# Kernel optimization log

Measured on AMD Instinct MI355X. Metric: run time of the kernel, lower is better.

## Reference

```python
import jax, jax.numpy as jnp
import numpy as np

D_MODEL = 1024
NUM_HEADS = 16
D_K = D_MODEL // NUM_HEADS
B, S = 4, 2048


def setup_inputs() -> dict:
    key = jax.random.key(0)
    ks = jax.random.split(key, 11)
    scale = 1.0 / np.sqrt(D_MODEL)
    inp = {
        'query': jax.random.normal(ks[0], (B, S, D_MODEL), dtype=jnp.float32),
        'key':   jax.random.normal(ks[1], (B, S, D_MODEL), dtype=jnp.float32),
        'value': jax.random.normal(ks[2], (B, S, D_MODEL), dtype=jnp.float32),
        'Wq': jax.random.normal(ks[3], (D_MODEL, D_MODEL), dtype=jnp.float32) * scale,
        'bq': jnp.zeros((D_MODEL,), dtype=jnp.float32),
        'Wk': jax.random.normal(ks[4], (D_MODEL, D_MODEL), dtype=jnp.float32) * scale,
        'bk': jnp.zeros((D_MODEL,), dtype=jnp.float32),
        'Wv': jax.random.normal(ks[5], (D_MODEL, D_MODEL), dtype=jnp.float32) * scale,
        'bv': jnp.zeros((D_MODEL,), dtype=jnp.float32),
        'Wo': jax.random.normal(ks[6], (D_MODEL, D_MODEL), dtype=jnp.float32) * scale,
        'bo': jnp.zeros((D_MODEL,), dtype=jnp.float32),
    }
    return inp


def reference(query, key, value, Wq, bq, Wk, bk, Wv, bv, Wo, bo):
    b, sq, _ = query.shape
    sk = key.shape[1]
    # projections (torch Linear: x @ W.T + b; here W stored as [in, out])
    Q = query @ Wq + bq
    K = key @ Wk + bk
    V = value @ Wv + bv
    # split heads: [b, h, s, d_k]
    Q = Q.reshape(b, sq, NUM_HEADS, D_K).transpose(0, 2, 1, 3)
    K = K.reshape(b, sk, NUM_HEADS, D_K).transpose(0, 2, 1, 3)
    V = V.reshape(b, sk, NUM_HEADS, D_K).transpose(0, 2, 1, 3)
    # scaled dot-product attention (full [b,h,sq,sk] scores, as in source)
    scores = jnp.einsum('bhqd,bhkd->bhqk', Q, K) / jnp.sqrt(jnp.float32(D_K))
    attn = jax.nn.softmax(scores, axis=-1)
    out = jnp.einsum('bhqk,bhkd->bhqd', attn, V)
    out = out.transpose(0, 2, 1, 3).reshape(b, sq, D_MODEL)
    return out @ Wo + bo
```

## Files before the change

### kernel.cpp

```cpp
#include <hip/hip_runtime.h>
#include <hip/hip_bf16.h>
#include <stdint.h>

typedef __bf16 bf16x8 __attribute__((ext_vector_type(8)));
typedef __bf16 bf16x4 __attribute__((ext_vector_type(4)));
typedef float  f32x4  __attribute__((ext_vector_type(4)));
typedef unsigned short u16;

#define D_MODEL 1024
#define NUM_HEADS 16
#define DK 64
#define BATCH 4
#define SEQ 2048
#define M_TOTAL (BATCH*SEQ)
#define QK_SCALE 0.18033688011112042f

static __device__ __forceinline__ u16 f2bf(float f) {
    __bf16 h = (__bf16)f;
    return __builtin_bit_cast(u16, h);
}

#define ASYNC16(gptr, lptr) __builtin_amdgcn_global_load_lds( \
    (const __attribute__((address_space(1))) unsigned*)(uintptr_t)(gptr), \
    (__attribute__((address_space(3))) unsigned*)(unsigned)(uintptr_t)(lptr), 16, 0, 0)

__global__ void detect_dtype(const u16* __restrict__ q, unsigned* __restrict__ flag) {
    __shared__ int sh[256];
    int cnt = 0;
    for (int i = threadIdx.x; i < 8192; i += 256) {
        u16 v = q[2 * i];
        int e = (v >> 7) & 0xFF;
        if (e >= 100 && e <= 134) cnt++;
    }
    sh[threadIdx.x] = cnt;
    __syncthreads();
    for (int s = 128; s > 0; s >>= 1) {
        if (threadIdx.x < s) sh[threadIdx.x] += sh[threadIdx.x + s];
        __syncthreads();
    }
    if (threadIdx.x == 0) *flag = (sh[0] > 4096) ? 1u : 0u;
}

__global__ void transpose_w(const u16* __restrict__ W0, const u16* __restrict__ W1,
                            const u16* __restrict__ W2, const u16* __restrict__ W3,
                            u16* __restrict__ WT, const unsigned* __restrict__ flagp) {
    __shared__ u16 tile[32][33];
    const u16* W = (blockIdx.z == 0) ? W0 : (blockIdx.z == 1) ? W1 : (blockIdx.z == 2) ? W2 : W3;
    u16* T = WT + (size_t)blockIdx.z * D_MODEL * D_MODEL;
    bool is_bf16 = (*flagp != 0);
    int x = threadIdx.x, y0 = threadIdx.y;
    int bx = blockIdx.x * 32, by = blockIdx.y * 32;
    if (is_bf16) {
#pragma unroll
        for (int i = 0; i < 4; i++) {
            int y = y0 + i * 8;
            tile[y][x] = W[(size_t)(by + y) * D_MODEL + bx + x];
        }
    } else {
        const float* Wf = (const float*)W;
#pragma unroll
        for (int i = 0; i < 4; i++) {
            int y = y0 + i * 8;
            tile[y][x] = f2bf(Wf[(size_t)(by + y) * D_MODEL + bx + x]);
        }
    }
    __syncthreads();
#pragma unroll
    for (int i = 0; i < 4; i++) {
        int y = y0 + i * 8;
        T[(size_t)(bx + y) * D_MODEL + by + x] = tile[x][y];
    }
}

__global__ __launch_bounds__(256) void gemm_qkv(
    const u16* __restrict__ qin, const u16* __restrict__ kin, const u16* __restrict__ vin,
    const u16* __restrict__ WT,
    const u16* __restrict__ bq, const u16* __restrict__ bk, const u16* __restrict__ bv,
    u16* __restrict__ Qp, u16* __restrict__ Kp, u16* __restrict__ VpT,
    const unsigned* __restrict__ flagp)
{
    __shared__ __align__(16) u16 As[128 * 32];
    __shared__ __align__(16) u16 Bs[128 * 32];
    const int id  = blockIdx.x;
    const int xcd = id & 7, j = id >> 3;
    const int zy  = xcd * 24 + (j >> 3);
    const int bx  = j & 7;
    const int z   = zy >> 6, by = zy & 63;

    const u16* A    = (z == 0) ? qin : (z == 1) ? kin : vin;
    const u16* W    = WT + (size_t)z * 1048576;
    const u16* bias = (z == 0) ? bq : (z == 1) ? bk : bv;
    u16* C          = (z == 0) ? Qp : (z == 1) ? Kp : VpT;
    const int transV = (z == 2);
    const float oscale = (z == 0) ? QK_SCALE : 1.0f;

    const int tid  = threadIdx.x;
    const int lane = tid & 63, w = tid >> 6;
    const int quad = lane >> 4, l15 = lane & 15;
    const int wm = w >> 1, wn = w & 1;
    const int m_blk = by * 128, n_blk = bx * 128;
    const bool is_bf16 = (*flagp != 0);

    f32x4 acc[4][4] = {};

    const int ch0 = w * 2, ch1 = w * 2 + 1;
    const int sr0 = ch0 * 16 + (lane >> 2), sr1 = ch1 * 16 + (lane >> 2);
    const int skp = (lane & 3) * 8;
    const int frow = tid >> 1, fkp = (tid & 1) * 16;
    const float* Af = (const float*)A;

    for (int k0 = 0; k0 < D_MODEL; k0 += 32) {
        if (!is_bf16) {
            const float* src = Af + (size_t)(m_blk + frow) * D_MODEL + k0 + fkp;
            float4 f0 = ((const float4*)src)[0];
            float4 f1 = ((const float4*)src)[1];
            float4 f2 = ((const float4*)src)[2];
            float4 f3 = ((const float4*)src)[3];
            bf16x8 p0, p1;
            p0[0] = (__bf16)f0.x; p0[1] = (__bf16)f0.y; p0[2] = (__bf16)f0.z; p0[3] = (__bf16)f0.w;
            p0[4] = (__bf16)f1.x; p0[5] = (__bf16)f1.y; p0[6] = (__bf16)f1.z; p0[7] = (__bf16)f1.w;
            p1[0] = (__bf16)f2.x; p1[1] = (__bf16)f2.y; p1[2] = (__bf16)f2.z; p1[3] = (__bf16)f2.w;
            p1[4] = (__bf16)f3.x; p1[5] = (__bf16)f3.y; p1[6] = (__bf16)f3.z; p1[7] = (__bf16)f3.w;
            *(bf16x8*)&As[frow * 32 + fkp]     = p0;
            *(bf16x8*)&As[frow * 32 + fkp + 8] = p1;
        } else {
            ASYNC16(A + (size_t)(m_blk + sr0) * D_MODEL + k0 + skp, &As[ch0 * 512]);
            ASYNC16(A + (size_t)(m_blk + sr1) * D_MODEL + k0 + skp, &As[ch1 * 512]);
        }
        ASYNC16(W + (size_t)(n_blk + sr0) * D_MODEL + k0 + skp, &Bs[ch0 * 512]);
        ASYNC16(W + (size_t)(n_blk + sr1) * D_MODEL + k0 + skp, &Bs[ch1 * 512]);
        __syncthreads();

        bf16x8 af[4], bg[4];
#pragma unroll
        for (int sm = 0; sm < 4; sm++)
            af[sm] = *(const bf16x8*)&As[(wm * 64 + sm * 16 + l15) * 32 + quad * 8];
#pragma unroll
        for (int sn = 0; sn < 4; sn++)
            bg[sn] = *(const bf16x8*)&Bs[(wn * 64 + sn * 16 + l15) * 32 + quad * 8];
#pragma unroll
        for (int sm = 0; sm < 4; sm++)
#pragma unroll
            for (int sn = 0; sn < 4; sn++)
                acc[sm][sn] = __builtin_amdgcn_mfma_f32_16x16x32_bf16(af[sm], bg[sn], acc[sm][sn], 0, 0, 0);
        __syncthreads();
    }

#pragma unroll
    for (int sn = 0; sn < 4; sn++) {
        int n = n_blk + wn * 64 + sn * 16 + l15;
        float bvf = is_bf16 ? (float)((const __bf16*)bias)[n] : ((const float*)bias)[n];
#pragma unroll
        for (int sm = 0; sm < 4; sm++) {
            int mrow = m_blk + wm * 64 + sm * 16 + quad * 4;
            if (transV) {
                int b = mrow >> 11, s = mrow & 2047;
                ushort4 pk;
                pk.x = f2bf(acc[sm][sn][0] + bvf);
                pk.y = f2bf(acc[sm][sn][1] + bvf);
                pk.z = f2bf(acc[sm][sn][2] + bvf);
                pk.w = f2bf(acc[sm][sn][3] + bvf);
                *(ushort4*)(C + (size_t)b * D_MODEL * SEQ + (size_t)n * SEQ + s) = pk;
            } else {
#pragma unroll
                for (int r = 0; r < 4; r++)
                    C[(size_t)(mrow + r) * D_MODEL + n] = f2bf((acc[sm][sn][r] + bvf) * oscale);
            }
        }
    }
}

__global__ __launch_bounds__(256) void gemm_o(
    const u16* __restrict__ A, const u16* __restrict__ WT,
    const u16* __restrict__ bias, u16* __restrict__ C,
    const unsigned* __restrict__ flagp)
{
    __shared__ __align__(16) u16 As[64 * 32];
    __shared__ __align__(16) u16 Bs[128 * 32];
    const int id  = blockIdx.x;
    const int xcd = id & 7, j = id >> 3;
    const int by  = xcd * 16 + (j >> 3);
    const int bx  = j & 7;

    const int tid  = threadIdx.x;
    const int lane = tid & 63, w = tid >> 6;
    const int quad = lane >> 4, l15 = lane & 15;
    const int wm = w >> 1, wn = w & 1;
    const int m_blk = by * 64, n_blk = bx * 128;
    const bool is_bf16 = (*flagp != 0);

    f32x4 acc[2][4] = {};
    const int srow = lane >> 2, skp = (lane & 3) * 8;

    for (int k0 = 0; k0 < D_MODEL; k0 += 32) {
#pragma unroll
        for (int i = 0; i < 3; i++) {
            int c = w * 3 + i;
            if (c < 4)
                ASYNC16(A  + (size_t)(m_blk + c * 16 + srow) * D_MODEL + k0 + skp, &As[c * 512]);
            else
                ASYNC16(WT + (size_t)(n_blk + (c - 4) * 16 + srow) * D_MODEL + k0 + skp, &Bs[(c - 4) * 512]);
        }
        __syncthreads();

        bf16x8 af[2], bg[4];
#pragma unroll
        for (int sm = 0; sm < 2; sm++)
            af[sm] = *(const bf16x8*)&As[(wm * 32 + sm * 16 + l15) * 32 + quad * 8];
#pragma unroll
        for (int sn = 0; sn < 4; sn++)
            bg[sn] = *(const bf16x8*)&Bs[(wn * 64 + sn * 16 + l15) * 32 + quad * 8];
#pragma unroll
        for (int sm = 0; sm < 2; sm++)
#pragma unroll
            for (int sn = 0; sn < 4; sn++)
                acc[sm][sn] = __builtin_amdgcn_mfma_f32_16x16x32_bf16(af[sm], bg[sn], acc[sm][sn], 0, 0, 0);
        __syncthreads();
    }

#pragma unroll
    for (int sn = 0; sn < 4; sn++) {
        int n = n_blk + wn * 64 + sn * 16 + l15;
        float bvf = is_bf16 ? (float)((const __bf16*)bias)[n] : ((const float*)bias)[n];
#pragma unroll
        for (int sm = 0; sm < 2; sm++) {
            int mrow = m_blk + wm * 32 + sm * 16 + quad * 4;
            if (!is_bf16) {
                float* Cf = (float*)C;
#pragma unroll
                for (int r = 0; r < 4; r++)
                    Cf[(size_t)(mrow + r) * D_MODEL + n] = acc[sm][sn][r] + bvf;
            } else {
#pragma unroll
                for (int r = 0; r < 4; r++)
                    C[(size_t)(mrow + r) * D_MODEL + n] = f2bf(acc[sm][sn][r] + bvf);
            }
        }
    }
}

__global__ __launch_bounds__(256) void attn_kernel(
    const u16* __restrict__ Qp, const u16* __restrict__ Kp,
    const u16* __restrict__ VpT, u16* __restrict__ AO)
{
    __shared__ __align__(16) u16 Ks[2][64 * 64];
    __shared__ __align__(16) u16 Vs[2][64 * 64];
    __shared__ __align__(16) u16 Ps[4][32][68];
    const int id  = blockIdx.x;
    const int xcd = id & 7, j = id >> 3;
    const int bh  = xcd * 8 + (j >> 4);
    const int qx  = j & 15;

    const int tid  = threadIdx.x;
    const int lane = tid & 63, w = tid >> 6;
    const int quad = lane >> 4, l15 = lane & 15;
    const int b = bh >> 4, h = bh & 15;
    const int q_base = qx * 128 + w * 32;

    bf16x8 bQ[2][2];
#pragma unroll
    for (int sn = 0; sn < 2; sn++)
#pragma unroll
        for (int ds = 0; ds < 2; ds++)
            bQ[sn][ds] = *(const bf16x8*)(Qp + (size_t)(b * SEQ + q_base + sn * 16 + l15) * D_MODEL
                                              + h * DK + ds * 32 + quad * 8);

    float lsum[2] = {0.0f, 0.0f};
    f32x4 OT[2][4] = {};

    const u16* Kbase = Kp  + (size_t)(b * SEQ) * D_MODEL + h * DK;
    const u16* Vbase = VpT + (size_t)b * D_MODEL * SEQ + (size_t)(h * DK) * SEQ;

    const int c0   = w * 2;
    const int lrow = lane >> 3;
    const int ug   = (lane & 7) ^ lrow;
    const int swz  = l15 & 7;

    auto issue_tile = [&](int key0, int bf) {
#pragma unroll
        for (int i = 0; i < 2; i++) {
            int c = c0 + i;
            ASYNC16(Kbase + (size_t)(key0 + c * 8 + lrow) * D_MODEL + ug * 8, &Ks[bf][c * 512]);
            ASYNC16(Vbase + (size_t)(c * 8 + lrow) * SEQ + key0 + ug * 8,     &Vs[bf][c * 512]);
        }
    };

    issue_tile(0, 0);
    __syncthreads();

    for (int t = 0; t < SEQ / 64; t++) {
        const int cur = t & 1;
        if (t + 1 < SEQ / 64) issue_tile((t + 1) * 64, cur ^ 1);

#pragma unroll
        for (int kc = 0; kc < 4; kc++) {
            const int krow = (kc * 16 + l15) * 64;
            bf16x8 k0 = *(const bf16x8*)&Ks[cur][krow + ((quad ^ swz) * 8)];
            bf16x8 k1 = *(const bf16x8*)&Ks[cur][krow + (((4 + quad) ^ swz) * 8)];
#pragma unroll
            for (int sn = 0; sn < 2; sn++) {
                f32x4 s = {};
                s = __builtin_amdgcn_mfma_f32_16x16x32_bf16(k0, bQ[sn][0], s, 0, 0, 0);
                s = __builtin_amdgcn_mfma_f32_16x16x32_bf16(k1, bQ[sn][1], s, 0, 0, 0);
                float p0 = __builtin_amdgcn_exp2f(s[0]);
                float p1 = __builtin_amdgcn_exp2f(s[1]);
                float p2 = __builtin_amdgcn_exp2f(s[2]);
                float p3 = __builtin_amdgcn_exp2f(s[3]);
                lsum[sn] += (p0 + p1) + (p2 + p3);
                bf16x4 pk;
                pk[0] = (__bf16)p0; pk[1] = (__bf16)p1; pk[2] = (__bf16)p2; pk[3] = (__bf16)p3;
                *(bf16x4*)&Ps[w][sn * 16 + l15][kc * 16 + quad * 4] = pk;
            }
        }

#pragma unroll
        for (int kc2 = 0; kc2 < 2; kc2++) {
            bf16x8 bP0 = *(const bf16x8*)&Ps[w][l15][kc2 * 32 + quad * 8];
            bf16x8 bP1 = *(const bf16x8*)&Ps[w][16 + l15][kc2 * 32 + quad * 8];
#pragma unroll
            for (int nd = 0; nd < 4; nd++) {
                bf16x8 aV = *(const bf16x8*)&Vs[cur][(nd * 16 + l15) * 64
                                                    + (((kc2 * 4 + quad) ^ swz) * 8)];
                OT[0][nd] = __builtin_amdgcn_mfma_f32_16x16x32_bf16(aV, bP0, OT[0][nd], 0, 0, 0);
                OT[1][nd] = __builtin_amdgcn_mfma_f32_16x16x32_bf16(aV, bP1, OT[1][nd], 0, 0, 0);
            }
        }
        __syncthreads();
    }

#pragma unroll
    for (int sn = 0; sn < 2; sn++) {
        lsum[sn] += __shfl_xor(lsum[sn], 16, 64);
        lsum[sn] += __shfl_xor(lsum[sn], 32, 64);
        float rl = 1.0f / lsum[sn];
        size_t rowbase = (size_t)(b * SEQ + q_base + sn * 16 + l15) * D_MODEL + h * DK;
#pragma unroll
        for (int nd = 0; nd < 4; nd++) {
            ushort4 pk;
            pk.x = f2bf(OT[sn][nd][0] * rl);
            pk.y = f2bf(OT[sn][nd][1] * rl);
            pk.z = f2bf(OT[sn][nd][2] * rl);
            pk.w = f2bf(OT[sn][nd][3] * rl);
            *(ushort4*)(AO + rowbase + nd * 16 + quad * 4) = pk;
        }
    }
}

extern "C" void kernel_launch(void* const* d_in, const int* in_sizes, int n_in,
                              void* d_out, int out_size, void* d_ws, size_t ws_size,
                              hipStream_t stream) {
    const u16* q  = (const u16*)d_in[0];
    const u16* k  = (const u16*)d_in[1];
    const u16* v  = (const u16*)d_in[2];
    const u16* Wq = (const u16*)d_in[3];
    const u16* bq = (const u16*)d_in[4];
    const u16* Wk = (const u16*)d_in[5];
    const u16* bk = (const u16*)d_in[6];
    const u16* Wv = (const u16*)d_in[7];
    const u16* bv = (const u16*)d_in[8];
    const u16* Wo = (const u16*)d_in[9];
    const u16* bo = (const u16*)d_in[10];

    u16* ws   = (u16*)d_ws;
    unsigned* flagp = (unsigned*)ws;
    u16* WT   = ws + 16;
    u16* Qp   = WT + (size_t)4 * 1024 * 1024;
    u16* Kp   = Qp + (size_t)M_TOTAL * D_MODEL;
    u16* VpT  = Kp + (size_t)M_TOTAL * D_MODEL;
    u16* AO   = VpT + (size_t)M_TOTAL * D_MODEL;

    detect_dtype<<<1, 256, 0, stream>>>(q, flagp);
    transpose_w<<<dim3(32, 32, 4), dim3(32, 8), 0, stream>>>(Wq, Wk, Wv, Wo, WT, flagp);
    gemm_qkv<<<1536, 256, 0, stream>>>(q, k, v, WT, bq, bk, bv, Qp, Kp, VpT, flagp);
    attn_kernel<<<1024, 256, 0, stream>>>(Qp, Kp, VpT, AO);
    gemm_o<<<1024, 256, 0, stream>>>(AO, WT + 3 * 1048576, bo, (u16*)d_out, flagp);
}
```

Baseline: 417.7 us.

## Restructure QKV GEMM into 256x256 double-buffered ping-pong pipeline with swizzled LDS

Replaces the 128x128, single-buffered QKV projection GEMM with a 512-thread kernel that computes 256x256 output tiles. It uses a K-step of 64, double-buffered LDS with an XOR swizzle, and interleaves staging of the next tiles between quarter-blocks of MFMA work. Manual waitcnt/barrier control and s_setprio aim to overlap global loads with matrix math and raise operand reuse per LDS byte. The trade-offs are 128KB of LDS per block, which likely limits residency to one block per CU, and a 384-block grid that leaves an uneven final wave. The fp32 input path still converts synchronously in registers.

```diff
diff --git a/kernel.cpp b/kernel.cpp
--- a/kernel.cpp
+++ b/kernel.cpp
@@ -23,6 +23,9 @@
 #define ASYNC16(gptr, lptr) __builtin_amdgcn_global_load_lds( \
     (const __attribute__((address_space(1))) unsigned*)(uintptr_t)(gptr), \
     (__attribute__((address_space(3))) unsigned*)(unsigned)(uintptr_t)(lptr), 16, 0, 0)
+
+#define FENCE() asm volatile("" ::: "memory")
+#define BARRIER() do { FENCE(); __builtin_amdgcn_s_barrier(); FENCE(); } while (0)
 
 __global__ void detect_dtype(const u16* __restrict__ q, unsigned* __restrict__ flag) {
     __shared__ int sh[256];
@@ -72,99 +75,169 @@
     }
 }
 
-__global__ __launch_bounds__(256) void gemm_qkv(
+__global__ __launch_bounds__(512, 2) void gemm_qkv(
     const u16* __restrict__ qin, const u16* __restrict__ kin, const u16* __restrict__ vin,
     const u16* __restrict__ WT,
     const u16* __restrict__ bq, const u16* __restrict__ bk, const u16* __restrict__ bv,
     u16* __restrict__ Qp, u16* __restrict__ Kp, u16* __restrict__ VpT,
     const unsigned* __restrict__ flagp)
 {
-    __shared__ __align__(16) u16 As[128 * 32];
-    __shared__ __align__(16) u16 Bs[128 * 32];
+    __shared__ __align__(16) u16 As[2][256 * 64];
+    __shared__ __align__(16) u16 Bs[2][256 * 64];
+
+    const int KTILES = D_MODEL / 64;
+
     const int id  = blockIdx.x;
-    const int xcd = id & 7, j = id >> 3;
-    const int zy  = xcd * 24 + (j >> 3);
-    const int bx  = j & 7;
-    const int z   = zy >> 6, by = zy & 63;
+    const int wg  = (id & 7) * 48 + (id >> 3);
+    const int z   = wg >> 7;
+    const int rr  = wg & 127;
+    const int m_blk = (rr >> 2) * 256;
+    const int n_blk = (rr & 3) * 256;
 
     const u16* A    = (z == 0) ? qin : (z == 1) ? kin : vin;
     const u16* W    = WT + (size_t)z * 1048576;
     const u16* bias = (z == 0) ? bq : (z == 1) ? bk : bv;
     u16* C          = (z == 0) ? Qp : (z == 1) ? Kp : VpT;
-    const int transV = (z == 2);
     const float oscale = (z == 0) ? QK_SCALE : 1.0f;
+    const bool is_bf16 = (*flagp != 0);
+    const float* Af = (const float*)A;
 
     const int tid  = threadIdx.x;
     const int lane = tid & 63, w = tid >> 6;
     const int quad = lane >> 4, l15 = lane & 15;
-    const int wm = w >> 1, wn = w & 1;
-    const int m_blk = by * 128, n_blk = bx * 128;
-    const bool is_bf16 = (*flagp != 0);
-
-    f32x4 acc[4][4] = {};
-
-    const int ch0 = w * 2, ch1 = w * 2 + 1;
-    const int sr0 = ch0 * 16 + (lane >> 2), sr1 = ch1 * 16 + (lane >> 2);
-    const int skp = (lane & 3) * 8;
-    const int frow = tid >> 1, fkp = (tid & 1) * 16;
-    const float* Af = (const float*)A;
-
-    for (int k0 = 0; k0 < D_MODEL; k0 += 32) {
-        if (!is_bf16) {
-            const float* src = Af + (size_t)(m_blk + frow) * D_MODEL + k0 + fkp;
-            float4 f0 = ((const float4*)src)[0];
-            float4 f1 = ((const float4*)src)[1];
-            float4 f2 = ((const float4*)src)[2];
-            float4 f3 = ((const float4*)src)[3];
-            bf16x8 p0, p1;
-            p0[0] = (__bf16)f0.x; p0[1] = (__bf16)f0.y; p0[2] = (__bf16)f0.z; p0[3] = (__bf16)f0.w;
-            p0[4] = (__bf16)f1.x; p0[5] = (__bf16)f1.y; p0[6] = (__bf16)f1.z; p0[7] = (__bf16)f1.w;
-            p1[0] = (__bf16)f2.x; p1[1] = (__bf16)f2.y; p1[2] = (__bf16)f2.z; p1[3] = (__bf16)f2.w;
-            p1[4] = (__bf16)f3.x; p1[5] = (__bf16)f3.y; p1[6] = (__bf16)f3.z; p1[7] = (__bf16)f3.w;
-            *(bf16x8*)&As[frow * 32 + fkp]     = p0;
-            *(bf16x8*)&As[frow * 32 + fkp + 8] = p1;
-        } else {
-            ASYNC16(A + (size_t)(m_blk + sr0) * D_MODEL + k0 + skp, &As[ch0 * 512]);
-            ASYNC16(A + (size_t)(m_blk + sr1) * D_MODEL + k0 + skp, &As[ch1 * 512]);
-        }
-        ASYNC16(W + (size_t)(n_blk + sr0) * D_MODEL + k0 + skp, &Bs[ch0 * 512]);
-        ASYNC16(W + (size_t)(n_blk + sr1) * D_MODEL + k0 + skp, &Bs[ch1 * 512]);
-        __syncthreads();
-
-        bf16x8 af[4], bg[4];
-#pragma unroll
-        for (int sm = 0; sm < 4; sm++)
-            af[sm] = *(const bf16x8*)&As[(wm * 64 + sm * 16 + l15) * 32 + quad * 8];
-#pragma unroll
-        for (int sn = 0; sn < 4; sn++)
-            bg[sn] = *(const bf16x8*)&Bs[(wn * 64 + sn * 16 + l15) * 32 + quad * 8];
-#pragma unroll
-        for (int sm = 0; sm < 4; sm++)
-#pragma unroll
-            for (int sn = 0; sn < 4; sn++)
-                acc[sm][sn] = __builtin_amdgcn_mfma_f32_16x16x32_bf16(af[sm], bg[sn], acc[sm][sn], 0, 0, 0);
-        __syncthreads();
-    }
-
-#pragma unroll
-    for (int sn = 0; sn < 4; sn++) {
-        int n = n_blk + wn * 64 + sn * 16 + l15;
-        float bvf = is_bf16 ? (float)((const __bf16*)bias)[n] : ((const float*)bias)[n];
-#pragma unroll
-        for (int sm = 0; sm < 4; sm++) {
-            int mrow = m_blk + wm * 64 + sm * 16 + quad * 4;
-            if (transV) {
-                int b = mrow >> 11, s = mrow & 2047;
+    const int swz  = l15 & 7;
+    const int wm = w >> 2, wn = w & 3;
+
+    const int lrow = lane >> 3;
+    const int ug   = (lane & 7) ^ lrow;
+
+    auto stageA = [&](int t, int h) {
+        if (t >= KTILES) return;
+        u16* ldsbase = &As[t & 1][h * 8192];
+        const int k0 = t * 64;
+#pragma unroll
+        for (int i = 0; i < 2; i++) {
+            const int c   = w * 2 + i;
+            const int row = m_blk + h * 128 + c * 8 + lrow;
+            if (is_bf16) {
+                ASYNC16(A + (size_t)row * D_MODEL + k0 + ug * 8, ldsbase + c * 512);
+            } else {
+                const float* s = Af + (size_t)row * D_MODEL + k0 + ug * 8;
+                float4 f0 = ((const float4*)s)[0];
+                float4 f1 = ((const float4*)s)[1];
+                bf16x8 p;
+                p[0] = (__bf16)f0.x; p[1] = (__bf16)f0.y; p[2] = (__bf16)f0.z; p[3] = (__bf16)f0.w;
+                p[4] = (__bf16)f1.x; p[5] = (__bf16)f1.y; p[6] = (__bf16)f1.z; p[7] = (__bf16)f1.w;
+                *(bf16x8*)(ldsbase + c * 512 + lane * 8) = p;
+            }
+        }
+    };
+    auto stageB = [&](int t, int h) {
+        if (t >= KTILES) return;
+        u16* ldsbase = &Bs[t & 1][h * 8192];
+        const int k0 = t * 64;
+#pragma unroll
+        for (int i = 0; i < 2; i++) {
+            const int c   = w * 2 + i;
+            const int row = n_blk + h * 128 + c * 8 + lrow;
+            ASYNC16(W + (size_t)row * D_MODEL + k0 + ug * 8, ldsbase + c * 512);
+        }
+    };
+
+    f32x4 acc[8][4] = {};
+    bf16x8 a[4][2];
+    bf16x8 b[4][2];
+
+#define LOAD_A(MBASE) \
+    _Pragma("unroll") \
+    for (int mf = 0; mf < 4; mf++) \
+        _Pragma("unroll") \
+        for (int ks = 0; ks < 2; ks++) \
+            a[mf][ks] = *(const bf16x8*)&Abuf[(wm * 128 + (MBASE + mf) * 16 + l15) * 64 \
+                                              + (((ks * 4 + quad) ^ swz) * 8)];
+#define LOAD_B(NBASE) \
+    _Pragma("unroll") \
+    for (int nf = 0; nf < 2; nf++) \
+        _Pragma("unroll") \
+        for (int ks = 0; ks < 2; ks++) \
+            b[NBASE + nf][ks] = *(const bf16x8*)&Bbuf[(wn * 64 + (NBASE + nf) * 16 + l15) * 64 \
+                                                      + (((ks * 4 + quad) ^ swz) * 8)];
+#define MFMA_QUAD(MBASE, NBASE) \
+    __builtin_amdgcn_s_setprio(1); \
+    _Pragma("unroll") \
+    for (int mf = 0; mf < 4; mf++) \
+        _Pragma("unroll") \
+        for (int nf = 0; nf < 2; nf++) \
+            _Pragma("unroll") \
+            for (int ks = 0; ks < 2; ks++) \
+                acc[MBASE + mf][NBASE + nf] = __builtin_amdgcn_mfma_f32_16x16x32_bf16( \
+                    a[mf][ks], b[NBASE + nf][ks], acc[MBASE + mf][NBASE + nf], 0, 0, 0); \
+    __builtin_amdgcn_s_setprio(0);
+
+    stageB(0, 0); stageB(0, 1);
+    stageA(0, 0); stageA(0, 1);
+    stageB(1, 0); stageB(1, 1);
+    asm volatile("s_waitcnt vmcnt(4) lgkmcnt(0)" ::: "memory");
+    __builtin_amdgcn_s_barrier();
+    FENCE();
+
+#pragma unroll 1
+    for (int t = 0; t < KTILES; t++) {
+        const u16* Abuf = &As[t & 1][0];
+        const u16* Bbuf = &Bs[t & 1][0];
+
+        LOAD_A(0); LOAD_B(0);
+        stageA(t + 1, 0);
+        BARRIER();
+        asm volatile("s_waitcnt lgkmcnt(0)" ::: "memory");
+        MFMA_QUAD(0, 0);
+        BARRIER();
+
+        LOAD_B(2);
+        stageA(t + 1, 1);
+        BARRIER();
+        asm volatile("s_waitcnt lgkmcnt(0)" ::: "memory");
+        MFMA_QUAD(0, 2);
+        BARRIER();
+
+        LOAD_A(4);
+        stageB(t + 2, 0);
+        BARRIER();
+        asm volatile("s_waitcnt lgkmcnt(0)" ::: "memory");
+        MFMA_QUAD(4, 2);
+        BARRIER();
+
+        stageB(t + 2, 1);
+        BARRIER();
+        asm volatile("s_waitcnt lgkmcnt(0)" ::: "memory");
+        MFMA_QUAD(4, 0);
+        if (t == KTILES - 2)      { asm volatile("s_waitcnt vmcnt(0)" ::: "memory"); }
+        else if (t < KTILES - 2)  { asm volatile("s_waitcnt vmcnt(4)" ::: "memory"); }
+        BARRIER();
+    }
+#undef LOAD_A
+#undef LOAD_B
+#undef MFMA_QUAD
+
+#pragma unroll
+    for (int nf = 0; nf < 4; nf++) {
+        const int n = n_blk + wn * 64 + nf * 16 + l15;
+        const float bvf = is_bf16 ? (float)((const __bf16*)bias)[n] : ((const float*)bias)[n];
+#pragma unroll
+        for (int mf = 0; mf < 8; mf++) {
+            const int mrow = m_blk + wm * 128 + mf * 16 + quad * 4;
+            if (z == 2) {
+                const int bb = mrow >> 11, s = mrow & 2047;
                 ushort4 pk;
-                pk.x = f2bf(acc[sm][sn][0] + bvf);
-                pk.y = f2bf(acc[sm][sn][1] + bvf);
-                pk.z = f2bf(acc[sm][sn][2] + bvf);
-                pk.w = f2bf(acc[sm][sn][3] + bvf);
-                *(ushort4*)(C + (size_t)b * D_MODEL * SEQ + (size_t)n * SEQ + s) = pk;
+                pk.x = f2bf(acc[mf][nf][0] + bvf);
+                pk.y = f2bf(acc[mf][nf][1] + bvf);
+                pk.z = f2bf(acc[mf][nf][2] + bvf);
+                pk.w = f2bf(acc[mf][nf][3] + bvf);
+                *(ushort4*)(C + (size_t)bb * D_MODEL * SEQ + (size_t)n * SEQ + s) = pk;
             } else {
 #pragma unroll
                 for (int r = 0; r < 4; r++)
-                    C[(size_t)(mrow + r) * D_MODEL + n] = f2bf((acc[sm][sn][r] + bvf) * oscale);
+                    C[(size_t)(mrow + r) * D_MODEL + n] = f2bf((acc[mf][nf][r] + bvf) * oscale);
             }
         }
     }
@@ -371,7 +444,7 @@
 
     detect_dtype<<<1, 256, 0, stream>>>(q, flagp);
     transpose_w<<<dim3(32, 32, 4), dim3(32, 8), 0, stream>>>(Wq, Wk, Wv, Wo, WT, flagp);
-    gemm_qkv<<<1536, 256, 0, stream>>>(q, k, v, WT, bq, bk, bv, Qp, Kp, VpT, flagp);
+    gemm_qkv<<<384, 512, 0, stream>>>(q, k, v, WT, bq, bk, bv, Qp, Kp, VpT, flagp);
     attn_kernel<<<1024, 256, 0, stream>>>(Qp, Kp, VpT, AO);
     gemm_o<<<1024, 256, 0, stream>>>(AO, WT + 3 * 1048576, bo, (u16*)d_out, flagp);
 }
```

Result: slower. 443.2 us (+6.1%).

## Pre-convert fp32 activations to bf16 and widen QKV GEMM K-tile with swizzled LDS

Applied to the files above, without the earlier changes.

Adds a separate kernel that converts the fp32 q/k/v inputs to bf16 once, so the QKV GEMM can always use async global-to-LDS loads instead of doing in-loop fp32 loads and conversions. The GEMM K-step grows from 32 to 64 with an XOR-swizzled LDS layout meant to avoid bank conflicts, and the block-to-tile mapping is changed. The cost is an extra pass over the activations with a bf16 round-trip through memory; the conversion buffer is reused as the attention output buffer.

```diff
diff --git a/kernel.cpp b/kernel.cpp
--- a/kernel.cpp
+++ b/kernel.cpp
@@ -13,6 +13,7 @@
 #define BATCH 4
 #define SEQ 2048
 #define M_TOTAL (BATCH*SEQ)
+#define MD ((size_t)M_TOTAL * D_MODEL)
 #define QK_SCALE 0.18033688011112042f
 
 static __device__ __forceinline__ u16 f2bf(float f) {
@@ -39,6 +40,25 @@
         __syncthreads();
     }
     if (threadIdx.x == 0) *flag = (sh[0] > 4096) ? 1u : 0u;
+}
+
+__global__ __launch_bounds__(256) void convert_bf16(
+    const u16* __restrict__ q, const u16* __restrict__ k, const u16* __restrict__ v,
+    u16* __restrict__ CVT, const unsigned* __restrict__ flagp)
+{
+    if (*flagp != 0) return;
+    const int z = blockIdx.y;
+    const float* src = (const float*)((z == 0) ? q : (z == 1) ? k : v);
+    u16* dst = CVT + (size_t)z * MD;
+    const size_t stride = (size_t)gridDim.x * 256 * 8;
+    for (size_t base = ((size_t)blockIdx.x * 256 + threadIdx.x) * 8; base < MD; base += stride) {
+        float4 f0 = *(const float4*)(src + base);
+        float4 f1 = *(const float4*)(src + base + 4);
+        bf16x8 p;
+        p[0] = (__bf16)f0.x; p[1] = (__bf16)f0.y; p[2] = (__bf16)f0.z; p[3] = (__bf16)f0.w;
+        p[4] = (__bf16)f1.x; p[5] = (__bf16)f1.y; p[6] = (__bf16)f1.z; p[7] = (__bf16)f1.w;
+        *(bf16x8*)(dst + base) = p;
+    }
 }
 
 __global__ void transpose_w(const u16* __restrict__ W0, const u16* __restrict__ W1,
@@ -74,97 +94,92 @@
 
 __global__ __launch_bounds__(256) void gemm_qkv(
     const u16* __restrict__ qin, const u16* __restrict__ kin, const u16* __restrict__ vin,
-    const u16* __restrict__ WT,
+    const u16* __restrict__ CVT, const u16* __restrict__ WT,
     const u16* __restrict__ bq, const u16* __restrict__ bk, const u16* __restrict__ bv,
     u16* __restrict__ Qp, u16* __restrict__ Kp, u16* __restrict__ VpT,
     const unsigned* __restrict__ flagp)
 {
-    __shared__ __align__(16) u16 As[128 * 32];
-    __shared__ __align__(16) u16 Bs[128 * 32];
+    __shared__ __align__(16) u16 As[128 * 64];
+    __shared__ __align__(16) u16 Bs[128 * 64];
+
     const int id  = blockIdx.x;
-    const int xcd = id & 7, j = id >> 3;
-    const int zy  = xcd * 24 + (j >> 3);
-    const int bx  = j & 7;
-    const int z   = zy >> 6, by = zy & 63;
-
-    const u16* A    = (z == 0) ? qin : (z == 1) ? kin : vin;
+    const int wg  = (id & 7) * 192 + (id >> 3);
+    const int z   = wg >> 9;
+    const int rr  = wg & 511;
+    const int m_blk = (rr >> 3) * 128;
+    const int n_blk = (rr & 7) * 128;
+
+    const bool is_bf16 = (*flagp != 0);
+    const u16* A = is_bf16 ? ((z == 0) ? qin : (z == 1) ? kin : vin)
+                           : (CVT + (size_t)z * MD);
     const u16* W    = WT + (size_t)z * 1048576;
     const u16* bias = (z == 0) ? bq : (z == 1) ? bk : bv;
     u16* C          = (z == 0) ? Qp : (z == 1) ? Kp : VpT;
-    const int transV = (z == 2);
     const float oscale = (z == 0) ? QK_SCALE : 1.0f;
 
     const int tid  = threadIdx.x;
     const int lane = tid & 63, w = tid >> 6;
     const int quad = lane >> 4, l15 = lane & 15;
+    const int swz  = l15 & 7;
     const int wm = w >> 1, wn = w & 1;
-    const int m_blk = by * 128, n_blk = bx * 128;
-    const bool is_bf16 = (*flagp != 0);
+
+    const int lrow = lane >> 3;
+    const int ug   = (lane & 7) ^ lrow;
 
     f32x4 acc[4][4] = {};
 
-    const int ch0 = w * 2, ch1 = w * 2 + 1;
-    const int sr0 = ch0 * 16 + (lane >> 2), sr1 = ch1 * 16 + (lane >> 2);
-    const int skp = (lane & 3) * 8;
-    const int frow = tid >> 1, fkp = (tid & 1) * 16;
-    const float* Af = (const float*)A;
-
-    for (int k0 = 0; k0 < D_MODEL; k0 += 32) {
-        if (!is_bf16) {
-            const float* src = Af + (size_t)(m_blk + frow) * D_MODEL + k0 + fkp;
-            float4 f0 = ((const float4*)src)[0];
-            float4 f1 = ((const float4*)src)[1];
-            float4 f2 = ((const float4*)src)[2];
-            float4 f3 = ((const float4*)src)[3];
-            bf16x8 p0, p1;
-            p0[0] = (__bf16)f0.x; p0[1] = (__bf16)f0.y; p0[2] = (__bf16)f0.z; p0[3] = (__bf16)f0.w;
-            p0[4] = (__bf16)f1.x; p0[5] = (__bf16)f1.y; p0[6] = (__bf16)f1.z; p0[7] = (__bf16)f1.w;
-            p1[0] = (__bf16)f2.x; p1[1] = (__bf16)f2.y; p1[2] = (__bf16)f2.z; p1[3] = (__bf16)f2.w;
-            p1[4] = (__bf16)f3.x; p1[5] = (__bf16)f3.y; p1[6] = (__bf16)f3.z; p1[7] = (__bf16)f3.w;
-            *(bf16x8*)&As[frow * 32 + fkp]     = p0;
-            *(bf16x8*)&As[frow * 32 + fkp + 8] = p1;
-        } else {
-            ASYNC16(A + (size_t)(m_blk + sr0) * D_MODEL + k0 + skp, &As[ch0 * 512]);
-            ASYNC16(A + (size_t)(m_blk + sr1) * D_MODEL + k0 + skp, &As[ch1 * 512]);
-        }
-        ASYNC16(W + (size_t)(n_blk + sr0) * D_MODEL + k0 + skp, &Bs[ch0 * 512]);
-        ASYNC16(W + (size_t)(n_blk + sr1) * D_MODEL + k0 + skp, &Bs[ch1 * 512]);
-        __syncthreads();
-
-        bf16x8 af[4], bg[4];
-#pragma unroll
-        for (int sm = 0; sm < 4; sm++)
-            af[sm] = *(const bf16x8*)&As[(wm * 64 + sm * 16 + l15) * 32 + quad * 8];
-#pragma unroll
-        for (int sn = 0; sn < 4; sn++)
-            bg[sn] = *(const bf16x8*)&Bs[(wn * 64 + sn * 16 + l15) * 32 + quad * 8];
-#pragma unroll
-        for (int sm = 0; sm < 4; sm++)
-#pragma unroll
-            for (int sn = 0; sn < 4; sn++)
-                acc[sm][sn] = __builtin_amdgcn_mfma_f32_16x16x32_bf16(af[sm], bg[sn], acc[sm][sn], 0, 0, 0);
-        __syncthreads();
-    }
-
-#pragma unroll
-    for (int sn = 0; sn < 4; sn++) {
-        int n = n_blk + wn * 64 + sn * 16 + l15;
-        float bvf = is_bf16 ? (float)((const __bf16*)bias)[n] : ((const float*)bias)[n];
-#pragma unroll
-        for (int sm = 0; sm < 4; sm++) {
-            int mrow = m_blk + wm * 64 + sm * 16 + quad * 4;
-            if (transV) {
-                int b = mrow >> 11, s = mrow & 2047;
+    for (int k0 = 0; k0 < D_MODEL; k0 += 64) {
+#pragma unroll
+        for (int i = 0; i < 4; i++) {
+            const int c = w * 4 + i;
+            ASYNC16(A + (size_t)(m_blk + c * 8 + lrow) * D_MODEL + k0 + ug * 8, &As[c * 512]);
+            ASYNC16(W + (size_t)(n_blk + c * 8 + lrow) * D_MODEL + k0 + ug * 8, &Bs[c * 512]);
+        }
+        __syncthreads();
+
+        bf16x8 a[4][2], b[4][2];
+#pragma unroll
+        for (int mf = 0; mf < 4; mf++)
+#pragma unroll
+            for (int ks = 0; ks < 2; ks++)
+                a[mf][ks] = *(const bf16x8*)&As[(size_t)(wm * 64 + mf * 16 + l15) * 64
+                                                + (((ks * 4 + quad) ^ swz) * 8)];
+#pragma unroll
+        for (int nf = 0; nf < 4; nf++)
+#pragma unroll
+            for (int ks = 0; ks < 2; ks++)
+                b[nf][ks] = *(const bf16x8*)&Bs[(size_t)(wn * 64 + nf * 16 + l15) * 64
+                                                + (((ks * 4 + quad) ^ swz) * 8)];
+#pragma unroll
+        for (int mf = 0; mf < 4; mf++)
+#pragma unroll
+            for (int nf = 0; nf < 4; nf++)
+#pragma unroll
+                for (int ks = 0; ks < 2; ks++)
+                    acc[mf][nf] = __builtin_amdgcn_mfma_f32_16x16x32_bf16(
+                        a[mf][ks], b[nf][ks], acc[mf][nf], 0, 0, 0);
+        __syncthreads();
+    }
+
+#pragma unroll
+    for (int nf = 0; nf < 4; nf++) {
+        const int n = n_blk + wn * 64 + nf * 16 + l15;
+        const float bvf = is_bf16 ? (float)((const __bf16*)bias)[n] : ((const float*)bias)[n];
+#pragma unroll
+        for (int mf = 0; mf < 4; mf++) {
+            const int mrow = m_blk + wm * 64 + mf * 16 + quad * 4;
+            if (z == 2) {
+                const int bb = mrow >> 11, s = mrow & 2047;
                 ushort4 pk;
-                pk.x = f2bf(acc[sm][sn][0] + bvf);
-                pk.y = f2bf(acc[sm][sn][1] + bvf);
-                pk.z = f2bf(acc[sm][sn][2] + bvf);
-                pk.w = f2bf(acc[sm][sn][3] + bvf);
-                *(ushort4*)(C + (size_t)b * D_MODEL * SEQ + (size_t)n * SEQ + s) = pk;
+                pk.x = f2bf(acc[mf][nf][0] + bvf);
+                pk.y = f2bf(acc[mf][nf][1] + bvf);
+                pk.z = f2bf(acc[mf][nf][2] + bvf);
+                pk.w = f2bf(acc[mf][nf][3] + bvf);
+                *(ushort4*)(C + (size_t)bb * D_MODEL * SEQ + (size_t)n * SEQ + s) = pk;
             } else {
 #pragma unroll
                 for (int r = 0; r < 4; r++)
-                    C[(size_t)(mrow + r) * D_MODEL + n] = f2bf((acc[sm][sn][r] + bvf) * oscale);
+                    C[(size_t)(mrow + r) * D_MODEL + n] = f2bf((acc[mf][nf][r] + bvf) * oscale);
             }
         }
     }
@@ -365,13 +380,15 @@
     unsigned* flagp = (unsigned*)ws;
     u16* WT   = ws + 16;
     u16* Qp   = WT + (size_t)4 * 1024 * 1024;
-    u16* Kp   = Qp + (size_t)M_TOTAL * D_MODEL;
-    u16* VpT  = Kp + (size_t)M_TOTAL * D_MODEL;
-    u16* AO   = VpT + (size_t)M_TOTAL * D_MODEL;
+    u16* Kp   = Qp + MD;
+    u16* VpT  = Kp + MD;
+    u16* CVT  = VpT + MD;
+    u16* AO   = CVT;
 
     detect_dtype<<<1, 256, 0, stream>>>(q, flagp);
+    convert_bf16<<<dim3(1024, 3), 256, 0, stream>>>(q, k, v, CVT, flagp);
     transpose_w<<<dim3(32, 32, 4), dim3(32, 8), 0, stream>>>(Wq, Wk, Wv, Wo, WT, flagp);
-    gemm_qkv<<<1536, 256, 0, stream>>>(q, k, v, WT, bq, bk, bv, Qp, Kp, VpT, flagp);
+    gemm_qkv<<<1536, 256, 0, stream>>>(q, k, v, CVT, WT, bq, bk, bv, Qp, Kp, VpT, flagp);
     attn_kernel<<<1024, 256, 0, stream>>>(Qp, Kp, VpT, AO);
     gemm_o<<<1024, 256, 0, stream>>>(AO, WT + 3 * 1048576, bo, (u16*)d_out, flagp);
 }
```

Measured after the change: 400.4 us. 4.1% less time.
